# Optimization experiments

Measured on AMD Instinct MI355X. Metric: run time of the kernel, lower is better.

## Reference

```python
import jax, jax.numpy as jnp
import numpy as np

N_MID = 100000
D = 64
B = 64
S = 256
K = 10
BIG_NEG = -2.0**32 + 1.0


def _din(q, facts, mask, W1, b1, W2, b2, W3, b3):
    # q broadcastable to facts shape; facts [..., T, D]; mask [..., T]
    qb = jnp.broadcast_to(q, facts.shape)
    x = jnp.concatenate([qb, facts, qb - facts, qb * facts], axis=-1)  # [..., T, 4D]
    h = jax.nn.sigmoid(x @ W1 + b1)
    h = jax.nn.sigmoid(h @ W2 + b2)
    s = (h @ W3 + b3)[..., 0]  # [..., T]
    s = jnp.where(mask == 1.0, s, BIG_NEG)
    a = jax.nn.softmax(s, axis=-1)
    return jnp.einsum('...t,...td->...d', a, facts)


def _prelu(x, alpha):
    return jnp.maximum(x, 0.0) + alpha * jnp.minimum(x, 0.0)


def setup_inputs():
    key = jax.random.key(0)
    ks = iter(jax.random.split(key, 48))
    def nrm(shape, scale=0.05):
        return jax.random.normal(next(ks), shape, dtype=jnp.float32) * scale
    inp = {}
    inp['mid'] = jax.random.randint(next(ks), (B,), 0, N_MID)
    inp['click_his'] = jax.random.randint(next(ks), (B, S), 0, N_MID)
    inp['unclick_his'] = jax.random.randint(next(ks), (B, K * S), 0, N_MID)
    inp['click_mask'] = jnp.ones((B, S), jnp.float32)
    inp['unclick_mask'] = jnp.ones((B, K * S), jnp.float32)
    inp['emb'] = nrm((N_MID, D), 0.1)
    for p in ('s', 'c', 'u'):  # search / click / unclick attention MLPs
        inp[p + 'W1'] = nrm((4 * D, 80)); inp[p + 'b1'] = jnp.zeros((80,), jnp.float32)
        inp[p + 'W2'] = nrm((80, 40));    inp[p + 'b2'] = jnp.zeros((40,), jnp.float32)
        inp[p + 'W3'] = nrm((40, 1));     inp[p + 'b3'] = jnp.zeros((1,), jnp.float32)
    F = 3 * D
    inp['bn_g'] = jnp.ones((F,), jnp.float32); inp['bn_b'] = jnp.zeros((F,), jnp.float32)
    inp['bn_m'] = jnp.zeros((F,), jnp.float32); inp['bn_v'] = jnp.ones((F,), jnp.float32)
    inp['fW1'] = nrm((F, 200)); inp['fb1'] = jnp.zeros((200,), jnp.float32); inp['a1'] = 0.25 * jnp.ones((200,), jnp.float32)
    inp['fW2'] = nrm((200, 80)); inp['fb2'] = jnp.zeros((80,), jnp.float32); inp['a2'] = 0.25 * jnp.ones((80,), jnp.float32)
    inp['fW3'] = nrm((80, 2)); inp['fb3'] = jnp.zeros((2,), jnp.float32)
    return inp


def reference(mid, click_his, unclick_his, click_mask, unclick_mask, emb,
              sW1, sb1, sW2, sb2, sW3, sb3,
              cW1, cb1, cW2, cb2, cW3, cb3,
              uW1, ub1, uW2, ub2, uW3, ub3,
              bn_g, bn_b, bn_m, bn_v,
              fW1, fb1, a1, fW2, fb2, a2, fW3, fb3):
    item = emb[mid]                                        # [B, D]
    click = emb[click_his] * click_mask[..., None]         # [B, S, D]
    unclick = emb[unclick_his] * unclick_mask[..., None]   # [B, K*S, D]
    uf = unclick.reshape(B, S, K, D)
    umask = unclick_mask.reshape(B, S, K)
    # din_attention_1: per clicked item, attend over its K unclicked items
    un_att = _din(click[:, :, None, :], uf, umask, sW1, sb1, sW2, sb2, sW3, sb3)  # [B, S, D]
    # denoise: project unclick rep onto click rep (shared component)
    dot = jnp.sum(un_att * click, axis=-1, keepdims=True)
    nrm2 = jnp.sum(click * click, axis=-1, keepdims=True) + 1e-12  # ||target||^2
    shared = dot * click / nrm2
    att1 = _din(item[:, None, :], click + shared, click_mask, cW1, cb1, cW2, cb2, cW3, cb3)  # [B, D]
    att2 = _din(item[:, None, :], un_att, click_mask, uW1, ub1, uW2, ub2, uW3, ub3)          # [B, D]
    x = jnp.concatenate([item, att1, att2], axis=-1)  # [B, 3D]
    x = (x - bn_m) / jnp.sqrt(bn_v + 1e-3) * bn_g + bn_b  # inference batchnorm
    x = _prelu(x @ fW1 + fb1, a1)
    x = _prelu(x @ fW2 + fb2, a2)
    logits = x @ fW3 + fb3
    return jax.nn.softmax(logits, axis=-1) + 1e-8
```

## Files before the change

### kernel.cpp

```cpp
#include <hip/hip_runtime.h>
#include <hip/hip_bf16.h>
#include <math.h>

#define BB 64
#define SS 256
#define KK 10
#define DD 64
#define FF 192
#define FH1 200
#define FH2 80
#define BIG_NEG_F (-4294967295.0f)

#define XSTR 200
#define H1STR 104

#define W1ELTS (80 * XSTR)
#define W2ELTS (48 * H1STR)
#define WREG   (W1ELTS + W2ELTS)

typedef __bf16 bfrag __attribute__((ext_vector_type(8)));
typedef float f32x4 __attribute__((ext_vector_type(4)));

__device__ __forceinline__ float sigm_(float x) { return 1.0f / (1.0f + __expf(-x)); }

__global__ __launch_bounds__(256) void k_prep(
    const float* __restrict__ sW1, const float* __restrict__ sW2,
    const float* __restrict__ cW1, const float* __restrict__ cW2,
    const float* __restrict__ uW1, const float* __restrict__ uW2,
    __bf16* __restrict__ Wt)
{
    const int p = blockIdx.x, g = blockIdx.y;
    const float* W1 = (p == 0) ? sW1 : (p == 1) ? cW1 : uW1;
    const float* W2 = (p == 0) ? sW2 : (p == 1) ? cW2 : uW2;
    __bf16* o1 = Wt + p * WREG;
    __bf16* o2 = o1 + W1ELTS;
    for (int e = g * 256 + threadIdx.x; e < 200 * 80; e += 2560) {
        const int k = e / 80, n = e % 80;
        float v;
        if (k < 64)       v = W1[k * 80 + n] + W1[(k + 128) * 80 + n];
        else if (k < 128) v = W1[k * 80 + n] - W1[(k + 64) * 80 + n];
        else if (k < 192) v = W1[(k + 64) * 80 + n];
        else              v = 0.0f;
        o1[n * XSTR + k] = (__bf16)v;
    }
    for (int e = g * 256 + threadIdx.x; e < W2ELTS; e += 2560) {
        const int n = e / H1STR, k = e % H1STR;
        o2[e] = (__bf16)((n < 40 && k < 80) ? W2[k * 40 + n] : 0.0f);
    }
}

__device__ __forceinline__ void mlp_core(
    const float* qv, const float* fv,
    const __bf16* __restrict__ sW1, __bf16* __restrict__ sH1w,
    const bfrag* wb2, const float* b1v, const float* b2v, const float* w3v,
    int quad, int l15, float* score)
{
    bfrag af[6];
    #pragma unroll
    for (int j = 0; j < 8; ++j) {
        af[0][j] = (__bf16)qv[j];
        af[1][j] = (__bf16)qv[8 + j];
        af[2][j] = (__bf16)fv[j];
        af[3][j] = (__bf16)fv[8 + j];
        af[4][j] = (__bf16)(qv[j] * fv[j]);
        af[5][j] = (__bf16)(qv[8 + j] * fv[8 + j]);
    }

    f32x4 acc[5];
    #pragma unroll
    for (int nt = 0; nt < 5; ++nt) acc[nt] = (f32x4){0.f, 0.f, 0.f, 0.f};
    {
        const __bf16* wbase = sW1 + l15 * XSTR + quad * 8;
        #pragma unroll
        for (int nt = 0; nt < 5; ++nt) {
            const __bf16* wp = wbase + nt * 16 * XSTR;
            #pragma unroll
            for (int kc = 0; kc < 6; ++kc)
                acc[nt] = __builtin_amdgcn_mfma_f32_16x16x32_bf16(
                    af[kc], *(const bfrag*)(wp + kc * 32), acc[nt], 0, 0, 0);
        }
    }

    #pragma unroll
    for (int nt = 0; nt < 5; ++nt) {
        #pragma unroll
        for (int rg = 0; rg < 4; ++rg)
            sH1w[(quad * 4 + rg) * H1STR + nt * 16 + l15] =
                (__bf16)sigm_(acc[nt][rg] + b1v[nt]);
    }
    #pragma unroll
    for (int rg = 0; rg < 4; ++rg)
        sH1w[(quad * 4 + rg) * H1STR + 80 + l15] = (__bf16)0.0f;

    bfrag af2[3];
    {
        const __bf16* hrow = sH1w + l15 * H1STR + quad * 8;
        #pragma unroll
        for (int kc = 0; kc < 3; ++kc) af2[kc] = *(const bfrag*)(hrow + kc * 32);
    }
    f32x4 acc2[3];
    #pragma unroll
    for (int nt = 0; nt < 3; ++nt) acc2[nt] = (f32x4){0.f, 0.f, 0.f, 0.f};
    #pragma unroll
    for (int nt = 0; nt < 3; ++nt)
        #pragma unroll
        for (int kc = 0; kc < 3; ++kc)
            acc2[nt] = __builtin_amdgcn_mfma_f32_16x16x32_bf16(
                af2[kc], wb2[nt * 3 + kc], acc2[nt], 0, 0, 0);

    float part[4] = {0.f, 0.f, 0.f, 0.f};
    #pragma unroll
    for (int nt = 0; nt < 3; ++nt) {
        #pragma unroll
        for (int rg = 0; rg < 4; ++rg)
            part[rg] += sigm_(acc2[nt][rg] + b2v[nt]) * w3v[nt];
    }
    #pragma unroll
    for (int off = 1; off < 16; off <<= 1) {
        #pragma unroll
        for (int rg = 0; rg < 4; ++rg)
            part[rg] += __shfl_xor(part[rg], off, 64);
    }
    #pragma unroll
    for (int rg = 0; rg < 4; ++rg) score[rg] = part[rg];
}

__global__ __launch_bounds__(320) void k_din0(
    const int* __restrict__ click_his, const int* __restrict__ unclick_his,
    const float* __restrict__ click_mask, const float* __restrict__ unclick_mask,
    const float* __restrict__ emb, const __bf16* __restrict__ Wt,
    const float* __restrict__ b1, const float* __restrict__ b2,
    const float* __restrict__ W3, const float* __restrict__ b3,
    float* __restrict__ unatt, float* __restrict__ coef)
{
    __shared__ __align__(16) __bf16 sW1[80 * XSTR];
    __shared__ __align__(16) __bf16 sH1[5 * 16 * H1STR];
    __shared__ float ssc[80];

    const int t = threadIdx.x;
    const int wave = t >> 6, lane = t & 63;
    const int quad = lane >> 4, l15 = lane & 15;

    {
        const uint4* s1 = (const uint4*)Wt;
        uint4* d1 = (uint4*)sW1;
        for (int e = t; e < W1ELTS / 8; e += 320) d1[e] = s1[e];
    }

    bfrag wb2[9];
    float b1v[5], b2v[3], w3v[3];
    {
        const __bf16* w2g = Wt + W1ELTS;
        #pragma unroll
        for (int nt = 0; nt < 3; ++nt)
            #pragma unroll
            for (int kc = 0; kc < 3; ++kc)
                wb2[nt * 3 + kc] = *(const bfrag*)(w2g + (nt * 16 + l15) * H1STR + kc * 32 + quad * 8);
        #pragma unroll
        for (int nt = 0; nt < 5; ++nt) b1v[nt] = b1[nt * 16 + l15];
        #pragma unroll
        for (int nt = 0; nt < 3; ++nt) {
            const int n = nt * 16 + l15;
            b2v[nt] = (n < 40) ? b2[n] : 0.0f;
            w3v[nt] = (n < 40) ? W3[n] : 0.0f;
        }
    }
    const float b3v = b3[0];

    const int row = 16 * wave + l15;
    const int m   = blockIdx.x * 80 + row;
    const int bs  = blockIdx.x * 8 + row / 10;
    float qv[16], fv[16];
    {
        const float* qp = emb + (size_t)click_his[bs] * DD;
        const float* fp = emb + (size_t)unclick_his[m] * DD;
        const float qs = click_mask[bs], fs = unclick_mask[m];
        const int c = quad * 8;
        *(float4*)(qv + 0)  = *(const float4*)(qp + c);
        *(float4*)(qv + 4)  = *(const float4*)(qp + c + 4);
        *(float4*)(qv + 8)  = *(const float4*)(qp + 32 + c);
        *(float4*)(qv + 12) = *(const float4*)(qp + 32 + c + 4);
        *(float4*)(fv + 0)  = *(const float4*)(fp + c);
        *(float4*)(fv + 4)  = *(const float4*)(fp + c + 4);
        *(float4*)(fv + 8)  = *(const float4*)(fp + 32 + c);
        *(float4*)(fv + 12) = *(const float4*)(fp + 32 + c + 4);
        #pragma unroll
        for (int i = 0; i < 16; ++i) { qv[i] *= qs; fv[i] *= fs; }
    }
    __syncthreads();

    float score[4];
    mlp_core(qv, fv, sW1, sH1 + wave * 16 * H1STR, wb2, b1v, b2v, w3v, quad, l15, score);

    if (l15 == 0) {
        #pragma unroll
        for (int rg = 0; rg < 4; ++rg) {
            const int r2 = 16 * wave + quad * 4 + rg;
            const int m2 = blockIdx.x * 80 + r2;
            ssc[r2] = (unclick_mask[m2] == 1.0f) ? (score[rg] + b3v) : BIG_NEG_F;
        }
    }
    __syncthreads();

    for (int j = wave; j < 8; j += 5) {
        const int bsj = blockIdx.x * 8 + j;
        float a[KK];
        float mx = -INFINITY;
        #pragma unroll
        for (int k = 0; k < KK; ++k) { a[k] = ssc[j * KK + k]; mx = fmaxf(mx, a[k]); }
        float sum = 0.0f;
        #pragma unroll
        for (int k = 0; k < KK; ++k) { a[k] = __expf(a[k] - mx); sum += a[k]; }
        const float inv = 1.0f / sum;
        float acc3 = 0.0f;
        #pragma unroll
        for (int k = 0; k < KK; ++k) {
            const int off = bsj * KK + k;
            acc3 += a[k] * (emb[(size_t)unclick_his[off] * DD + lane] * unclick_mask[off]);
        }
        acc3 *= inv;
        unatt[(size_t)bsj * DD + lane] = acc3;
        const float qv2 = emb[(size_t)click_his[bsj] * DD + lane] * click_mask[bsj];
        float dp = acc3 * qv2, nq = qv2 * qv2;
        #pragma unroll
        for (int o = 32; o > 0; o >>= 1) {
            dp += __shfl_down(dp, o, 64);
            nq += __shfl_down(nq, o, 64);
        }
        if (lane == 0) coef[bsj] = 1.0f + dp / (nq + 1e-12f);
    }
}

__global__ __launch_bounds__(512) void k_din12(
    const int* __restrict__ mid, const int* __restrict__ click_his,
    const float* __restrict__ click_mask,
    const float* __restrict__ emb, const float* __restrict__ unatt,
    const float* __restrict__ coef, const __bf16* __restrict__ Wt,
    const float* __restrict__ cb1, const float* __restrict__ cb2,
    const float* __restrict__ cW3, const float* __restrict__ cb3,
    const float* __restrict__ ub1, const float* __restrict__ ub2,
    const float* __restrict__ uW3, const float* __restrict__ ub3,
    float* __restrict__ scores_c, float* __restrict__ scores_u)
{
    __shared__ __align__(16) __bf16 sW1[80 * XSTR];
    __shared__ __align__(16) __bf16 sH1[8][16 * H1STR];

    const int t = threadIdx.x;
    const int mode = blockIdx.y;
    const int wave = t >> 6, lane = t & 63;
    const int quad = lane >> 4, l15 = lane & 15;

    const float* b1 = mode ? ub1 : cb1;
    const float* b2 = mode ? ub2 : cb2;
    const float* W3 = mode ? uW3 : cW3;
    const float* b3 = mode ? ub3 : cb3;
    const __bf16* wreg = Wt + (mode + 1) * WREG;

    {
        const uint4* s1 = (const uint4*)wreg;
        uint4* d1 = (uint4*)sW1;
        for (int e = t; e < W1ELTS / 8; e += 512) d1[e] = s1[e];
    }

    bfrag wb2[9];
    float b1v[5], b2v[3], w3v[3];
    {
        const __bf16* w2g = wreg + W1ELTS;
        #pragma unroll
        for (int nt = 0; nt < 3; ++nt)
            #pragma unroll
            for (int kc = 0; kc < 3; ++kc)
                wb2[nt * 3 + kc] = *(const bfrag*)(w2g + (nt * 16 + l15) * H1STR + kc * 32 + quad * 8);
        #pragma unroll
        for (int nt = 0; nt < 5; ++nt) b1v[nt] = b1[nt * 16 + l15];
        #pragma unroll
        for (int nt = 0; nt < 3; ++nt) {
            const int n = nt * 16 + l15;
            b2v[nt] = (n < 40) ? b2[n] : 0.0f;
            w3v[nt] = (n < 40) ? W3[n] : 0.0f;
        }
    }
    const float b3v = b3[0];

    const int row = 16 * wave + l15;
    const int m   = blockIdx.x * 128 + row;
    const int b   = m >> 8;
    float qv[16], fv[16];
    {
        const float* qp = emb + (size_t)mid[b] * DD;
        const float* fp; float fs;
        if (mode == 0) { fp = emb + (size_t)click_his[m] * DD; fs = click_mask[m] * coef[m]; }
        else           { fp = unatt + (size_t)m * DD; fs = 1.0f; }
        const int c = quad * 8;
        *(float4*)(qv + 0)  = *(const float4*)(qp + c);
        *(float4*)(qv + 4)  = *(const float4*)(qp + c + 4);
        *(float4*)(qv + 8)  = *(const float4*)(qp + 32 + c);
        *(float4*)(qv + 12) = *(const float4*)(qp + 32 + c + 4);
        *(float4*)(fv + 0)  = *(const float4*)(fp + c);
        *(float4*)(fv + 4)  = *(const float4*)(fp + c + 4);
        *(float4*)(fv + 8)  = *(const float4*)(fp + 32 + c);
        *(float4*)(fv + 12) = *(const float4*)(fp + 32 + c + 4);
        #pragma unroll
        for (int i = 0; i < 16; ++i) fv[i] *= fs;
    }
    __syncthreads();

    float score[4];
    mlp_core(qv, fv, sW1, sH1[wave], wb2, b1v, b2v, w3v, quad, l15, score);

    if (l15 == 0) {
        float* dst = mode ? scores_u : scores_c;
        #pragma unroll
        for (int rg = 0; rg < 4; ++rg) {
            const int m2 = blockIdx.x * 128 + 16 * wave + quad * 4 + rg;
            dst[m2] = (click_mask[m2] == 1.0f) ? (score[rg] + b3v) : BIG_NEG_F;
        }
    }
}

__global__ __launch_bounds__(1024) void k_tail(
    const int* __restrict__ mid, const int* __restrict__ click_his,
    const float* __restrict__ click_mask,
    const float* __restrict__ emb, const float* __restrict__ unatt,
    const float* __restrict__ coef,
    const float* __restrict__ scores_c, const float* __restrict__ scores_u,
    const float* __restrict__ bn_g, const float* __restrict__ bn_b,
    const float* __restrict__ bn_m, const float* __restrict__ bn_v,
    const float* __restrict__ fW1, const float* __restrict__ fb1, const float* __restrict__ a1,
    const float* __restrict__ fW2, const float* __restrict__ fb2, const float* __restrict__ a2,
    const float* __restrict__ fW3, const float* __restrict__ fb3,
    float* __restrict__ out)
{
    const int b = blockIdx.x, t = threadIdx.x;
    const int wave = t >> 6, lane = t & 63;
    const int ty = wave >> 3, w8 = wave & 7;
    const int s0 = w8 * 32;

    __shared__ float sa[2][SS];
    __shared__ float smax[16], ssum[16];
    __shared__ float part[16][72];
    __shared__ float x[FF];
    __shared__ float ph1[4][FH1];
    __shared__ float h1s[FH1];
    __shared__ float ph2[8][FH2];
    __shared__ float h2s[FH2];
    __shared__ float red2[2];

    if (t < DD) x[t] = emb[(size_t)mid[b] * DD + t];

    const float* scp = ty ? scores_u : scores_c;
    const float sc = (lane < 32) ? scp[b * SS + s0 + lane] : -INFINITY;
    float mloc = sc;
    #pragma unroll
    for (int o = 32; o > 0; o >>= 1) mloc = fmaxf(mloc, __shfl_xor(mloc, o, 64));
    if (lane == 0) smax[wave] = mloc;
    __syncthreads();

    float mt = smax[ty * 8];
    #pragma unroll
    for (int i = 1; i < 8; ++i) mt = fmaxf(mt, smax[ty * 8 + i]);
    const float e = (lane < 32) ? __expf(sc - mt) : 0.0f;
    if (lane < 32) sa[ty][s0 + lane] = e;
    float sloc = e;
    #pragma unroll
    for (int o = 32; o > 0; o >>= 1) sloc += __shfl_xor(sloc, o, 64);
    if (lane == 0) ssum[wave] = sloc;
    __syncthreads();

    float den = 0.0f;
    #pragma unroll
    for (int i = 0; i < 8; ++i) den += ssum[ty * 8 + i];
    const float inv = 1.0f / den;

    float acc = 0.0f;
    #pragma unroll 8
    for (int i = 0; i < 32; ++i) {
        const int s2 = s0 + i;
        const int bs = b * SS + s2;
        const float fv = ty ? unatt[(size_t)bs * DD + lane]
                            : emb[(size_t)click_his[bs] * DD + lane] * click_mask[bs] * coef[bs];
        acc += sa[ty][s2] * fv;
    }
    part[wave][lane] = acc * inv;
    __syncthreads();

    if (t < 128) {
        const int tt = t >> 6, d = t & 63;
        float v = 0.0f;
        #pragma unroll
        for (int i = 0; i < 8; ++i) v += part[tt * 8 + i][d];
        x[DD + tt * DD + d] = v;
    }
    __syncthreads();

    if (t < FF) x[t] = (x[t] - bn_m[t]) * rsqrtf(bn_v[t] + 1e-3f) * bn_g[t] + bn_b[t];
    __syncthreads();

    if (t < 800) {
        const int n = t % FH1, cc = t / FH1;
        float p = 0.0f;
        #pragma unroll 8
        for (int i = cc * 48; i < cc * 48 + 48; ++i) p += x[i] * fW1[i * FH1 + n];
        ph1[cc][n] = p;
    }
    __syncthreads();
    if (t < FH1) {
        const float a = ph1[0][t] + ph1[1][t] + ph1[2][t] + ph1[3][t] + fb1[t];
        h1s[t] = fmaxf(a, 0.0f) + a1[t] * fminf(a, 0.0f);
    }
    __syncthreads();

    if (t < 640) {
        const int n = t % FH2, cc = t / FH2;
        float p = 0.0f;
        #pragma unroll 5
        for (int i = cc * 25; i < cc * 25 + 25; ++i) p += h1s[i] * fW2[i * FH2 + n];
        ph2[cc][n] = p;
    }
    __syncthreads();
    if (t < FH2) {
        float a = fb2[t];
        #pragma unroll
        for (int cc = 0; cc < 8; ++cc) a += ph2[cc][t];
        h2s[t] = fmaxf(a, 0.0f) + a2[t] * fminf(a, 0.0f);
    }
    __syncthreads();

    if (t < 128) {
        const int o = t >> 6;
        float p = h2s[lane] * fW3[lane * 2 + o];
        if (lane < 16) p += h2s[64 + lane] * fW3[(64 + lane) * 2 + o];
        #pragma unroll
        for (int off = 32; off > 0; off >>= 1) p += __shfl_down(p, off, 64);
        if (lane == 0) red2[o] = p + fb3[o];
    }
    __syncthreads();
    if (t == 0) {
        const float l0 = red2[0], l1 = red2[1];
        const float mx = fmaxf(l0, l1);
        const float e0 = __expf(l0 - mx), e1 = __expf(l1 - mx);
        const float invs = 1.0f / (e0 + e1);
        out[b * 2 + 0] = e0 * invs + 1e-8f;
        out[b * 2 + 1] = e1 * invs + 1e-8f;
    }
}

extern "C" void kernel_launch(void* const* d_in, const int* in_sizes, int n_in,
                              void* d_out, int out_size, void* d_ws, size_t ws_size,
                              hipStream_t stream) {
    const int*   mid          = (const int*)d_in[0];
    const int*   click_his    = (const int*)d_in[1];
    const int*   unclick_his  = (const int*)d_in[2];
    const float* click_mask   = (const float*)d_in[3];
    const float* unclick_mask = (const float*)d_in[4];
    const float* emb          = (const float*)d_in[5];
    const float* sW1 = (const float*)d_in[6];  const float* sb1 = (const float*)d_in[7];
    const float* sW2 = (const float*)d_in[8];  const float* sb2 = (const float*)d_in[9];
    const float* sW3 = (const float*)d_in[10]; const float* sb3 = (const float*)d_in[11];
    const float* cW1 = (const float*)d_in[12]; const float* cb1 = (const float*)d_in[13];
    const float* cW2 = (const float*)d_in[14]; const float* cb2 = (const float*)d_in[15];
    const float* cW3 = (const float*)d_in[16]; const float* cb3 = (const float*)d_in[17];
    const float* uW1 = (const float*)d_in[18]; const float* ub1 = (const float*)d_in[19];
    const float* uW2 = (const float*)d_in[20]; const float* ub2 = (const float*)d_in[21];
    const float* uW3 = (const float*)d_in[22]; const float* ub3 = (const float*)d_in[23];
    const float* bn_g = (const float*)d_in[24]; const float* bn_b = (const float*)d_in[25];
    const float* bn_m = (const float*)d_in[26]; const float* bn_v = (const float*)d_in[27];
    const float* fW1 = (const float*)d_in[28]; const float* fb1 = (const float*)d_in[29];
    const float* a1  = (const float*)d_in[30];
    const float* fW2 = (const float*)d_in[31]; const float* fb2 = (const float*)d_in[32];
    const float* a2  = (const float*)d_in[33];
    const float* fW3 = (const float*)d_in[34]; const float* fb3 = (const float*)d_in[35];

    float* out = (float*)d_out;

    char* w = (char*)d_ws;
    __bf16* Wt      = (__bf16*)(w + 0);
    float* scores_c = (float*)(w + 125952);
    float* scores_u = (float*)(w + 191488);
    float* coef     = (float*)(w + 257024);
    float* unatt    = (float*)(w + 322560);

    hipLaunchKernelGGL(k_prep, dim3(3, 10), dim3(256), 0, stream,
        sW1, sW2, cW1, cW2, uW1, uW2, Wt);

    hipLaunchKernelGGL(k_din0, dim3(2048), dim3(320), 0, stream,
        click_his, unclick_his, click_mask, unclick_mask, emb, Wt,
        sb1, sb2, sW3, sb3, unatt, coef);

    hipLaunchKernelGGL(k_din12, dim3(128, 2), dim3(512), 0, stream,
        mid, click_his, click_mask, emb, unatt, coef, Wt,
        cb1, cb2, cW3, cb3, ub1, ub2, uW3, ub3, scores_c, scores_u);

    hipLaunchKernelGGL(k_tail, dim3(BB), dim3(1024), 0, stream,
        mid, click_his, click_mask, emb, unatt, coef, scores_c, scores_u,
        bn_g, bn_b, bn_m, bn_v, fW1, fb1, a1, fW2, fb2, a2, fW3, fb3, out);
}
```

Baseline: 222.5 us.

## Fuse attention-score MLP and tail into one per-batch kernel

Merges the k_din12 score kernel and the k_tail softmax/pooling/final-MLP kernel into a single kernel with one 512-thread block per batch row. Scores stay in shared memory instead of a global round trip, and one launch is removed. The tail's scratch buffers alias the MLP hidden-activation shared buffer. Also widens the weight-prep grid. In exchange, parallelism drops from 256 blocks to 64, each block loads both weight sets serially, and the tail MLPs run with fewer threads.

```diff
diff --git a/kernel.cpp b/kernel.cpp
--- a/kernel.cpp
+++ b/kernel.cpp
@@ -34,7 +34,7 @@
     const float* W2 = (p == 0) ? sW2 : (p == 1) ? cW2 : uW2;
     __bf16* o1 = Wt + p * WREG;
     __bf16* o2 = o1 + W1ELTS;
-    for (int e = g * 256 + threadIdx.x; e < 200 * 80; e += 2560) {
+    for (int e = g * 256 + threadIdx.x; e < 200 * 80; e += 10240) {
         const int k = e / 80, n = e % 80;
         float v;
         if (k < 64)       v = W1[k * 80 + n] + W1[(k + 128) * 80 + n];
@@ -43,7 +43,7 @@
         else              v = 0.0f;
         o1[n * XSTR + k] = (__bf16)v;
     }
-    for (int e = g * 256 + threadIdx.x; e < W2ELTS; e += 2560) {
+    for (int e = g * 256 + threadIdx.x; e < W2ELTS; e += 10240) {
         const int n = e / H1STR, k = e % H1STR;
         o2[e] = (__bf16)((n < 40 && k < 80) ? W2[k * 40 + n] : 0.0f);
     }
@@ -231,7 +231,7 @@
     }
 }
 
-__global__ __launch_bounds__(512) void k_din12(
+__global__ __launch_bounds__(512) void k_fused(
     const int* __restrict__ mid, const int* __restrict__ click_his,
     const float* __restrict__ click_mask,
     const float* __restrict__ emb, const float* __restrict__ unatt,
@@ -240,90 +240,6 @@
     const float* __restrict__ cW3, const float* __restrict__ cb3,
     const float* __restrict__ ub1, const float* __restrict__ ub2,
     const float* __restrict__ uW3, const float* __restrict__ ub3,
-    float* __restrict__ scores_c, float* __restrict__ scores_u)
-{
-    __shared__ __align__(16) __bf16 sW1[80 * XSTR];
-    __shared__ __align__(16) __bf16 sH1[8][16 * H1STR];
-
-    const int t = threadIdx.x;
-    const int mode = blockIdx.y;
-    const int wave = t >> 6, lane = t & 63;
-    const int quad = lane >> 4, l15 = lane & 15;
-
-    const float* b1 = mode ? ub1 : cb1;
-    const float* b2 = mode ? ub2 : cb2;
-    const float* W3 = mode ? uW3 : cW3;
-    const float* b3 = mode ? ub3 : cb3;
-    const __bf16* wreg = Wt + (mode + 1) * WREG;
-
-    {
-        const uint4* s1 = (const uint4*)wreg;
-        uint4* d1 = (uint4*)sW1;
-        for (int e = t; e < W1ELTS / 8; e += 512) d1[e] = s1[e];
-    }
-
-    bfrag wb2[9];
-    float b1v[5], b2v[3], w3v[3];
-    {
-        const __bf16* w2g = wreg + W1ELTS;
-        #pragma unroll
-        for (int nt = 0; nt < 3; ++nt)
-            #pragma unroll
-            for (int kc = 0; kc < 3; ++kc)
-                wb2[nt * 3 + kc] = *(const bfrag*)(w2g + (nt * 16 + l15) * H1STR + kc * 32 + quad * 8);
-        #pragma unroll
-        for (int nt = 0; nt < 5; ++nt) b1v[nt] = b1[nt * 16 + l15];
-        #pragma unroll
-        for (int nt = 0; nt < 3; ++nt) {
-            const int n = nt * 16 + l15;
-            b2v[nt] = (n < 40) ? b2[n] : 0.0f;
-            w3v[nt] = (n < 40) ? W3[n] : 0.0f;
-        }
-    }
-    const float b3v = b3[0];
-
-    const int row = 16 * wave + l15;
-    const int m   = blockIdx.x * 128 + row;
-    const int b   = m >> 8;
-    float qv[16], fv[16];
-    {
-        const float* qp = emb + (size_t)mid[b] * DD;
-        const float* fp; float fs;
-        if (mode == 0) { fp = emb + (size_t)click_his[m] * DD; fs = click_mask[m] * coef[m]; }
-        else           { fp = unatt + (size_t)m * DD; fs = 1.0f; }
-        const int c = quad * 8;
-        *(float4*)(qv + 0)  = *(const float4*)(qp + c);
-        *(float4*)(qv + 4)  = *(const float4*)(qp + c + 4);
-        *(float4*)(qv + 8)  = *(const float4*)(qp + 32 + c);
-        *(float4*)(qv + 12) = *(const float4*)(qp + 32 + c + 4);
-        *(float4*)(fv + 0)  = *(const float4*)(fp + c);
-        *(float4*)(fv + 4)  = *(const float4*)(fp + c + 4);
-        *(float4*)(fv + 8)  = *(const float4*)(fp + 32 + c);
-        *(float4*)(fv + 12) = *(const float4*)(fp + 32 + c + 4);
-        #pragma unroll
-        for (int i = 0; i < 16; ++i) fv[i] *= fs;
-    }
-    __syncthreads();
-
-    float score[4];
-    mlp_core(qv, fv, sW1, sH1[wave], wb2, b1v, b2v, w3v, quad, l15, score);
-
-    if (l15 == 0) {
-        float* dst = mode ? scores_u : scores_c;
-        #pragma unroll
-        for (int rg = 0; rg < 4; ++rg) {
-            const int m2 = blockIdx.x * 128 + 16 * wave + quad * 4 + rg;
-            dst[m2] = (click_mask[m2] == 1.0f) ? (score[rg] + b3v) : BIG_NEG_F;
-        }
-    }
-}
-
-__global__ __launch_bounds__(1024) void k_tail(
-    const int* __restrict__ mid, const int* __restrict__ click_his,
-    const float* __restrict__ click_mask,
-    const float* __restrict__ emb, const float* __restrict__ unatt,
-    const float* __restrict__ coef,
-    const float* __restrict__ scores_c, const float* __restrict__ scores_u,
     const float* __restrict__ bn_g, const float* __restrict__ bn_b,
     const float* __restrict__ bn_m, const float* __restrict__ bn_v,
     const float* __restrict__ fW1, const float* __restrict__ fb1, const float* __restrict__ a1,
@@ -331,97 +247,169 @@
     const float* __restrict__ fW3, const float* __restrict__ fb3,
     float* __restrict__ out)
 {
+    __shared__ __align__(16) __bf16 sW1[80 * XSTR];
+    __shared__ __align__(16) __bf16 sH1[8][16 * H1STR];
+    __shared__ float ssc[2][SS];
+
     const int b = blockIdx.x, t = threadIdx.x;
     const int wave = t >> 6, lane = t & 63;
-    const int ty = wave >> 3, w8 = wave & 7;
-    const int s0 = w8 * 32;
-
-    __shared__ float sa[2][SS];
-    __shared__ float smax[16], ssum[16];
-    __shared__ float part[16][72];
-    __shared__ float x[FF];
-    __shared__ float ph1[4][FH1];
-    __shared__ float h1s[FH1];
-    __shared__ float ph2[8][FH2];
-    __shared__ float h2s[FH2];
-    __shared__ float red2[2];
-
-    if (t < DD) x[t] = emb[(size_t)mid[b] * DD + t];
-
-    const float* scp = ty ? scores_u : scores_c;
-    const float sc = (lane < 32) ? scp[b * SS + s0 + lane] : -INFINITY;
-    float mloc = sc;
-    #pragma unroll
-    for (int o = 32; o > 0; o >>= 1) mloc = fmaxf(mloc, __shfl_xor(mloc, o, 64));
-    if (lane == 0) smax[wave] = mloc;
-    __syncthreads();
-
-    float mt = smax[ty * 8];
-    #pragma unroll
-    for (int i = 1; i < 8; ++i) mt = fmaxf(mt, smax[ty * 8 + i]);
-    const float e = (lane < 32) ? __expf(sc - mt) : 0.0f;
-    if (lane < 32) sa[ty][s0 + lane] = e;
-    float sloc = e;
-    #pragma unroll
-    for (int o = 32; o > 0; o >>= 1) sloc += __shfl_xor(sloc, o, 64);
-    if (lane == 0) ssum[wave] = sloc;
-    __syncthreads();
-
-    float den = 0.0f;
-    #pragma unroll
-    for (int i = 0; i < 8; ++i) den += ssum[ty * 8 + i];
-    const float inv = 1.0f / den;
-
-    float acc = 0.0f;
-    #pragma unroll 8
-    for (int i = 0; i < 32; ++i) {
-        const int s2 = s0 + i;
-        const int bs = b * SS + s2;
-        const float fv = ty ? unatt[(size_t)bs * DD + lane]
-                            : emb[(size_t)click_his[bs] * DD + lane] * click_mask[bs] * coef[bs];
-        acc += sa[ty][s2] * fv;
-    }
-    part[wave][lane] = acc * inv;
-    __syncthreads();
-
-    if (t < 128) {
-        const int tt = t >> 6, d = t & 63;
-        float v = 0.0f;
-        #pragma unroll
-        for (int i = 0; i < 8; ++i) v += part[tt * 8 + i][d];
-        x[DD + tt * DD + d] = v;
-    }
-    __syncthreads();
-
-    if (t < FF) x[t] = (x[t] - bn_m[t]) * rsqrtf(bn_v[t] + 1e-3f) * bn_g[t] + bn_b[t];
-    __syncthreads();
-
-    if (t < 800) {
+    const int quad = lane >> 4, l15 = lane & 15;
+    const int c = quad * 8;
+
+    float* scratch = (float*)&sH1[0][0];
+    float* part = scratch;
+    float* xv   = scratch + 576;
+    float* ph1  = scratch + 768;
+    float* h1s  = scratch + 1168;
+    float* ph2  = scratch + 1368;
+    float* h2s  = scratch + 1768;
+    float* smax = scratch + 1848;
+    float* ssum = scratch + 1856;
+    float* red2 = scratch + 1864;
+
+    const float* qp = emb + (size_t)mid[b] * DD;
+    float qv[16];
+    *(float4*)(qv + 0)  = *(const float4*)(qp + c);
+    *(float4*)(qv + 4)  = *(const float4*)(qp + c + 4);
+    *(float4*)(qv + 8)  = *(const float4*)(qp + 32 + c);
+    *(float4*)(qv + 12) = *(const float4*)(qp + 32 + c + 4);
+
+    #pragma unroll 1
+    for (int mode = 0; mode < 2; ++mode) {
+        const __bf16* wreg = Wt + (mode + 1) * WREG;
+        {
+            const uint4* s1 = (const uint4*)wreg;
+            uint4* d1 = (uint4*)sW1;
+            for (int e = t; e < W1ELTS / 8; e += 512) d1[e] = s1[e];
+        }
+        bfrag wb2[9];
+        float b1v[5], b2v[3], w3v[3];
+        {
+            const float* b1 = mode ? ub1 : cb1;
+            const float* b2 = mode ? ub2 : cb2;
+            const float* W3 = mode ? uW3 : cW3;
+            const __bf16* w2g = wreg + W1ELTS;
+            #pragma unroll
+            for (int nt = 0; nt < 3; ++nt)
+                #pragma unroll
+                for (int kc = 0; kc < 3; ++kc)
+                    wb2[nt * 3 + kc] = *(const bfrag*)(w2g + (nt * 16 + l15) * H1STR + kc * 32 + quad * 8);
+            #pragma unroll
+            for (int nt = 0; nt < 5; ++nt) b1v[nt] = b1[nt * 16 + l15];
+            #pragma unroll
+            for (int nt = 0; nt < 3; ++nt) {
+                const int n = nt * 16 + l15;
+                b2v[nt] = (n < 40) ? b2[n] : 0.0f;
+                w3v[nt] = (n < 40) ? W3[n] : 0.0f;
+            }
+        }
+        const float b3v = (mode ? ub3 : cb3)[0];
+        __syncthreads();
+
+        #pragma unroll 1
+        for (int tt = 0; tt < 2; ++tt) {
+            const int row = wave * 32 + tt * 16 + l15;
+            const int m   = b * SS + row;
+            float fv[16];
+            {
+                const float* fp; float fs;
+                if (mode == 0) { fp = emb + (size_t)click_his[m] * DD; fs = click_mask[m] * coef[m]; }
+                else           { fp = unatt + (size_t)m * DD; fs = 1.0f; }
+                *(float4*)(fv + 0)  = *(const float4*)(fp + c);
+                *(float4*)(fv + 4)  = *(const float4*)(fp + c + 4);
+                *(float4*)(fv + 8)  = *(const float4*)(fp + 32 + c);
+                *(float4*)(fv + 12) = *(const float4*)(fp + 32 + c + 4);
+                #pragma unroll
+                for (int i = 0; i < 16; ++i) fv[i] *= fs;
+            }
+            float score[4];
+            mlp_core(qv, fv, sW1, sH1[wave], wb2, b1v, b2v, w3v, quad, l15, score);
+            if (l15 == 0) {
+                #pragma unroll
+                for (int rg = 0; rg < 4; ++rg) {
+                    const int r2 = wave * 32 + tt * 16 + quad * 4 + rg;
+                    const int m2 = b * SS + r2;
+                    ssc[mode][r2] = (click_mask[m2] == 1.0f) ? (score[rg] + b3v) : BIG_NEG_F;
+                }
+            }
+        }
+        __syncthreads();
+    }
+
+    if (t < DD) xv[t] = qp[t];
+
+    #pragma unroll 1
+    for (int ty = 0; ty < 2; ++ty) {
+        const float sc = (lane < 32) ? ssc[ty][wave * 32 + lane] : -INFINITY;
+        float mloc = sc;
+        #pragma unroll
+        for (int o = 32; o > 0; o >>= 1) mloc = fmaxf(mloc, __shfl_xor(mloc, o, 64));
+        if (lane == 0) smax[wave] = mloc;
+        __syncthreads();
+        float mt = smax[0];
+        #pragma unroll
+        for (int i = 1; i < 8; ++i) mt = fmaxf(mt, smax[i]);
+        const float e = (lane < 32) ? __expf(sc - mt) : 0.0f;
+        float sloc = e;
+        #pragma unroll
+        for (int o = 32; o > 0; o >>= 1) sloc += __shfl_xor(sloc, o, 64);
+        if (lane == 0) ssum[wave] = sloc;
+        if (lane < 32) ssc[ty][wave * 32 + lane] = e;
+        __syncthreads();
+        float den = 0.0f;
+        #pragma unroll
+        for (int i = 0; i < 8; ++i) den += ssum[i];
+        const float inv = 1.0f / den;
+
+        float acc = 0.0f;
+        #pragma unroll 4
+        for (int i = 0; i < 32; ++i) {
+            const int s2 = wave * 32 + i;
+            const int bs = b * SS + s2;
+            const float fvv = ty ? unatt[(size_t)bs * DD + lane]
+                                 : emb[(size_t)click_his[bs] * DD + lane] * click_mask[bs] * coef[bs];
+            acc += ssc[ty][s2] * fvv;
+        }
+        part[wave * 72 + lane] = acc * inv;
+        __syncthreads();
+        if (t < DD) {
+            float v = 0.0f;
+            #pragma unroll
+            for (int w2 = 0; w2 < 8; ++w2) v += part[w2 * 72 + t];
+            xv[DD + ty * DD + t] = v;
+        }
+        __syncthreads();
+    }
+
+    if (t < FF) xv[t] = (xv[t] - bn_m[t]) * rsqrtf(bn_v[t] + 1e-3f) * bn_g[t] + bn_b[t];
+    __syncthreads();
+
+    if (t < 400) {
         const int n = t % FH1, cc = t / FH1;
         float p = 0.0f;
         #pragma unroll 8
-        for (int i = cc * 48; i < cc * 48 + 48; ++i) p += x[i] * fW1[i * FH1 + n];
-        ph1[cc][n] = p;
+        for (int i = cc * 96; i < cc * 96 + 96; ++i) p += xv[i] * fW1[i * FH1 + n];
+        ph1[cc * FH1 + n] = p;
     }
     __syncthreads();
     if (t < FH1) {
-        const float a = ph1[0][t] + ph1[1][t] + ph1[2][t] + ph1[3][t] + fb1[t];
+        const float a = ph1[t] + ph1[FH1 + t] + fb1[t];
         h1s[t] = fmaxf(a, 0.0f) + a1[t] * fminf(a, 0.0f);
     }
     __syncthreads();
 
-    if (t < 640) {
+    if (t < 400) {
         const int n = t % FH2, cc = t / FH2;
         float p = 0.0f;
-        #pragma unroll 5
-        for (int i = cc * 25; i < cc * 25 + 25; ++i) p += h1s[i] * fW2[i * FH2 + n];
-        ph2[cc][n] = p;
+        #pragma unroll 8
+        for (int i = cc * 40; i < cc * 40 + 40; ++i) p += h1s[i] * fW2[i * FH2 + n];
+        ph2[cc * FH2 + n] = p;
     }
     __syncthreads();
     if (t < FH2) {
         float a = fb2[t];
         #pragma unroll
-        for (int cc = 0; cc < 8; ++cc) a += ph2[cc][t];
+        for (int cc = 0; cc < 5; ++cc) a += ph2[cc * FH2 + t];
         h2s[t] = fmaxf(a, 0.0f) + a2[t] * fminf(a, 0.0f);
     }
     __syncthreads();
@@ -474,24 +462,19 @@
     float* out = (float*)d_out;
 
     char* w = (char*)d_ws;
-    __bf16* Wt      = (__bf16*)(w + 0);
-    float* scores_c = (float*)(w + 125952);
-    float* scores_u = (float*)(w + 191488);
-    float* coef     = (float*)(w + 257024);
-    float* unatt    = (float*)(w + 322560);
-
-    hipLaunchKernelGGL(k_prep, dim3(3, 10), dim3(256), 0, stream,
+    __bf16* Wt   = (__bf16*)(w + 0);
+    float* coef  = (float*)(w + 125952);
+    float* unatt = (float*)(w + 191488);
+
+    hipLaunchKernelGGL(k_prep, dim3(3, 40), dim3(256), 0, stream,
         sW1, sW2, cW1, cW2, uW1, uW2, Wt);
 
     hipLaunchKernelGGL(k_din0, dim3(2048), dim3(320), 0, stream,
         click_his, unclick_his, click_mask, unclick_mask, emb, Wt,
         sb1, sb2, sW3, sb3, unatt, coef);
 
-    hipLaunchKernelGGL(k_din12, dim3(128, 2), dim3(512), 0, stream,
+    hipLaunchKernelGGL(k_fused, dim3(BB), dim3(512), 0, stream,
         mid, click_his, click_mask, emb, unatt, coef, Wt,
-        cb1, cb2, cW3, cb3, ub1, ub2, uW3, ub3, scores_c, scores_u);
-
-    hipLaunchKernelGGL(k_tail, dim3(BB), dim3(1024), 0, stream,
-        mid, click_his, click_mask, emb, unatt, coef, scores_c, scores_u,
+        cb1, cb2, cW3, cb3, ub1, ub2, uW3, ub3,
         bn_g, bn_b, bn_m, bn_v, fW1, fb1, a1, fW2, fb2, a2, fW3, fb3, out);
 }
```

After: 224.0 us. About the same (+0.7%).
